# Performance work log

Hardware: AMD Instinct MI355X
Metric: run time of the kernel (lower is better)

## Reference

```python
import jax, jax.numpy as jnp
import numpy as np

N = 12000       # nodes (Hi-C bins, max_num_nodes)
F_IN = 16       # number_genomic_annotations
HID = 4 * F_IN  # conv1 out = 64
NCLUST = 100    # n_clust
E = 384000      # edges (avg degree 32)


def setup_inputs() -> dict:
    key = jax.random.key(0)
    ks = jax.random.split(key, 8)
    x = jax.random.normal(ks[0], (N, F_IN), dtype=jnp.float32)
    edge_index = jax.random.randint(ks[1], (2, E), 0, N)
    edge_attr = jax.random.uniform(ks[2], (E,), dtype=jnp.float32)
    s1 = 1.0 / np.sqrt(F_IN)
    W1_rel = jax.random.uniform(ks[3], (HID, F_IN), minval=-s1, maxval=s1, dtype=jnp.float32)
    W1_root = jax.random.uniform(ks[4], (HID, F_IN), minval=-s1, maxval=s1, dtype=jnp.float32)
    b1 = jnp.zeros((HID,), jnp.float32)
    s2 = 1.0 / np.sqrt(HID)
    W2_rel = jax.random.uniform(ks[5], (NCLUST, HID), minval=-s2, maxval=s2, dtype=jnp.float32)
    W2_root = jax.random.uniform(ks[6], (NCLUST, HID), minval=-s2, maxval=s2, dtype=jnp.float32)
    b2 = jnp.zeros((NCLUST,), jnp.float32)
    return dict(x=x, edge_index=edge_index, edge_attr=edge_attr,
                W1_rel=W1_rel, W1_root=W1_root, b1=b1,
                W2_rel=W2_rel, W2_root=W2_root, b2=b2)


def _graph_conv(x, src, dst, ew, W_rel, W_root, b):
    # PyG GraphConv (aggr='add'): out = lin_rel(sum_j e_ji * x_j) + lin_root(x)
    msg = x[src] * ew[:, None]                       # [E, F]
    aggr = jax.ops.segment_sum(msg, dst, num_segments=N)  # [N, F]
    return aggr @ W_rel.T + b + x @ W_root.T


def reference(x, edge_index, edge_attr, W1_rel, W1_root, b1, W2_rel, W2_root, b2):
    src, dst = edge_index[0], edge_index[1]
    h = _graph_conv(x, src, dst, edge_attr, W1_rel, W1_root, b1)
    h = jax.nn.relu(h)  # dropout is identity in eval mode
    s_out = _graph_conv(h, src, dst, edge_attr, W2_rel, W2_root, b2)  # [N, NCLUST]

    # to_dense_adj (duplicate edges summed)
    adj = jnp.zeros((N, N), x.dtype).at[src, dst].add(edge_attr)  # [N, N]

    # dense_mincut_pool with S = x (as in the original forward), k = F_IN
    s_mc = jax.nn.softmax(x, axis=-1)      # [N, F_IN]
    as_ = adj @ s_mc                        # [N, F_IN]
    out_adj = s_mc.T @ as_                  # [F_IN, F_IN]
    mincut_num = jnp.trace(out_adj)
    d_flat = adj.sum(-1)                    # [N] degree
    mincut_den = jnp.einsum('ik,i,ik->', s_mc, d_flat, s_mc)  # trace(S^T D S)
    mc = -(mincut_num / mincut_den)

    ss = s_mc.T @ s_mc                      # [F_IN, F_IN]
    i_k = jnp.eye(F_IN, dtype=ss.dtype)
    o = jnp.linalg.norm(ss / jnp.linalg.norm(ss) - i_k / jnp.linalg.norm(i_k))

    return jax.nn.softmax(s_out, axis=-1), mc, o
```

## Files before the change

### kernel.cpp

```cpp
#include <hip/hip_runtime.h>
#include <math.h>

#define N_NODES 12000
#define F_INN 16
#define HIDD 64
#define NCLUST 100
#define NEDGE 384000
#define NBLK_N 47
#define CAP 96
#define EPT 4
#define NBLK_E 375
#define NBLK_F1 (N_NODES / 4)
#define NBLK_F2 (N_NODES / 8)

#define OFF_COUNT   0
#define OFF_SCAL    12000
#define ZERO_ELEMS  12002
#define OFF_SSPART  12004
#define OFF_NORM2   24036
#define OFF_W2TREL  36036
#define OFF_W2TROOT 42436
#define OFF_SMC     48836
#define OFF_H       240836
#define OFF_SRCW    1008836

__global__ void zero_kernel(int* __restrict__ ws) {
    int i = blockIdx.x * 256 + threadIdx.x;
    if (i < ZERO_ELEMS) ws[i] = 0;
}

__global__ void phase0_kernel(const float* __restrict__ x, const int* __restrict__ ei,
                              const float* __restrict__ ew, float* __restrict__ smc,
                              float* __restrict__ norm2, int* __restrict__ count,
                              int2* __restrict__ srcw, const float* __restrict__ W2_rel,
                              const float* __restrict__ W2_root, float* __restrict__ w2t_rel,
                              float* __restrict__ w2t_root) {
    __shared__ float fl[6400];
    int t = threadIdx.x;
    int b = blockIdx.x;
    if (b < NBLK_N) {
        int i = b * 256 + t;
        if (i >= N_NODES) return;
        const float4* xr = (const float4*)(x + i * 16);
        float4 r0 = xr[0], r1 = xr[1], r2 = xr[2], r3 = xr[3];
        float v[16] = {r0.x, r0.y, r0.z, r0.w, r1.x, r1.y, r1.z, r1.w,
                       r2.x, r2.y, r2.z, r2.w, r3.x, r3.y, r3.z, r3.w};
        float m = v[0];
#pragma unroll
        for (int k = 1; k < 16; ++k) m = fmaxf(m, v[k]);
        float s = 0.f;
#pragma unroll
        for (int k = 0; k < 16; ++k) { v[k] = __expf(v[k] - m); s += v[k]; }
        float inv = 1.f / s;
        float n2 = 0.f;
#pragma unroll
        for (int k = 0; k < 16; ++k) { v[k] *= inv; n2 += v[k] * v[k]; }
        float4* so = (float4*)(smc + i * 16);
        so[0] = make_float4(v[0], v[1], v[2], v[3]);
        so[1] = make_float4(v[4], v[5], v[6], v[7]);
        so[2] = make_float4(v[8], v[9], v[10], v[11]);
        so[3] = make_float4(v[12], v[13], v[14], v[15]);
        norm2[i] = n2;
    } else if (b < NBLK_N + NBLK_E) {
        int tid = (b - NBLK_N) * 256 + t;
        int e0 = tid * EPT;
        int4 sv = *(const int4*)(ei + e0);
        int4 dv = *(const int4*)(ei + NEDGE + e0);
        float4 wv = *(const float4*)(ew + e0);
        int s[EPT] = {sv.x, sv.y, sv.z, sv.w};
        int d[EPT] = {dv.x, dv.y, dv.z, dv.w};
        float w[EPT] = {wv.x, wv.y, wv.z, wv.w};
        int pos[EPT];
#pragma unroll
        for (int i = 0; i < EPT; ++i) pos[i] = atomicAdd(&count[d[i]], 1);
#pragma unroll
        for (int i = 0; i < EPT; ++i) {
            unsigned long long pv = ((unsigned long long)(unsigned)__float_as_int(w[i]) << 32) |
                                    (unsigned)s[i];
            __builtin_nontemporal_store(pv, (unsigned long long*)&srcw[d[i] * CAP + pos[i]]);
        }
    } else {
        const float* src = (b == NBLK_N + NBLK_E) ? W2_rel : W2_root;
        float* dst = (b == NBLK_N + NBLK_E) ? w2t_rel : w2t_root;
        for (int i = t; i < 6400; i += 256) fl[i] = src[i];
        __syncthreads();
        for (int j = t; j < 6400; j += 256) {
            int kk = j / 100, cl = j - kk * 100;
            dst[j] = fl[cl * 64 + kk];
        }
    }
}

__global__ void fused1_pass2_kernel(const float* __restrict__ x, const int2* __restrict__ srcw,
                                    const int* __restrict__ count, const float* __restrict__ W1_rel,
                                    const float* __restrict__ W1_root, const float* __restrict__ b1,
                                    float* __restrict__ h, const float* __restrict__ smc,
                                    float* __restrict__ sspart, const int* __restrict__ ei,
                                    const float* __restrict__ ew, const float* __restrict__ norm2,
                                    float* __restrict__ scal) {
    __shared__ float shm[4352];
    int t = threadIdx.x;
    int b = blockIdx.x;
    if (b < NBLK_F1) {
        float* wrelT  = shm;
        float* wrootT = shm + 1024;
        float* b1s    = shm + 2048;
        float* aggr   = shm + 2112;
        float* xs     = shm + 2176;
        for (int idx = t; idx < 1024; idx += 256) {
            int f = idx >> 4, k = idx & 15;
            wrelT[(k << 6) + f]  = W1_rel[idx];
            wrootT[(k << 6) + f] = W1_root[idx];
        }
        if (t < 64) b1s[t] = b1[t];
        int w = t >> 6, lane = t & 63;
        int j2 = lane >> 2;
        int q  = lane & 3;
        int n = b * 4 + w;
        int len = count[n];
        const int2* bucket = srcw + n * CAP;
        float4 acc4 = make_float4(0.f, 0.f, 0.f, 0.f);
        int k = 0;
        for (; k + 31 < len; k += 32) {
            int2 pa = bucket[k + j2];
            int2 pb = bucket[k + 16 + j2];
            float4 va = *(const float4*)(x + pa.x * 16 + q * 4);
            float4 vb = *(const float4*)(x + pb.x * 16 + q * 4);
            float wa = __int_as_float(pa.y), wb = __int_as_float(pb.y);
            acc4.x = fmaf(va.x, wa, acc4.x); acc4.y = fmaf(va.y, wa, acc4.y);
            acc4.z = fmaf(va.z, wa, acc4.z); acc4.w = fmaf(va.w, wa, acc4.w);
            acc4.x = fmaf(vb.x, wb, acc4.x); acc4.y = fmaf(vb.y, wb, acc4.y);
            acc4.z = fmaf(vb.z, wb, acc4.z); acc4.w = fmaf(vb.w, wb, acc4.w);
        }
        for (; k < len; k += 16) {
            if (k + j2 < len) {
                int2 p = bucket[k + j2];
                float4 v = *(const float4*)(x + p.x * 16 + q * 4);
                float wt = __int_as_float(p.y);
                acc4.x = fmaf(v.x, wt, acc4.x); acc4.y = fmaf(v.y, wt, acc4.y);
                acc4.z = fmaf(v.z, wt, acc4.z); acc4.w = fmaf(v.w, wt, acc4.w);
            }
        }
        acc4.x += __shfl_xor(acc4.x, 4);  acc4.y += __shfl_xor(acc4.y, 4);
        acc4.z += __shfl_xor(acc4.z, 4);  acc4.w += __shfl_xor(acc4.w, 4);
        acc4.x += __shfl_xor(acc4.x, 8);  acc4.y += __shfl_xor(acc4.y, 8);
        acc4.z += __shfl_xor(acc4.z, 8);  acc4.w += __shfl_xor(acc4.w, 8);
        acc4.x += __shfl_xor(acc4.x, 16); acc4.y += __shfl_xor(acc4.y, 16);
        acc4.z += __shfl_xor(acc4.z, 16); acc4.w += __shfl_xor(acc4.w, 16);
        acc4.x += __shfl_xor(acc4.x, 32); acc4.y += __shfl_xor(acc4.y, 32);
        acc4.z += __shfl_xor(acc4.z, 32); acc4.w += __shfl_xor(acc4.w, 32);
        if (j2 == 0) *(float4*)(aggr + w * 16 + q * 4) = acc4;
        if (lane < 16) xs[w * 16 + lane] = x[n * 16 + lane];
        __syncthreads();
        float o = b1s[lane];
#pragma unroll
        for (int kk = 0; kk < 16; ++kk)
            o = fmaf(aggr[w * 16 + kk], wrelT[(kk << 6) + lane],
                     fmaf(xs[w * 16 + kk], wrootT[(kk << 6) + lane], o));
        __builtin_nontemporal_store(fmaxf(o, 0.f), &h[n * 64 + lane]);
    } else if (b < NBLK_F1 + NBLK_N) {
        int bb = b - NBLK_F1;
        float* rows = shm;
        int n = bb * 256 + t;
        float* rp = rows + t * 17;
        if (n < N_NODES) {
            const float4* sr = (const float4*)(smc + n * 16);
            float4 a0 = sr[0], a1 = sr[1], a2v = sr[2], a3 = sr[3];
            rp[0] = a0.x;  rp[1] = a0.y;  rp[2] = a0.z;  rp[3] = a0.w;
            rp[4] = a1.x;  rp[5] = a1.y;  rp[6] = a1.z;  rp[7] = a1.w;
            rp[8] = a2v.x; rp[9] = a2v.y; rp[10] = a2v.z; rp[11] = a2v.w;
            rp[12] = a3.x; rp[13] = a3.y; rp[14] = a3.z; rp[15] = a3.w;
        } else {
#pragma unroll
            for (int k = 0; k < 16; ++k) rp[k] = 0.f;
        }
        __syncthreads();
        int a = t & 15, bq = t >> 4;
        float accs = 0.f;
#pragma unroll 4
        for (int r = 0; r < 256; ++r)
            accs = fmaf(rows[r * 17 + a], rows[r * 17 + bq], accs);
        sspart[bb * 256 + t] = accs;
    } else {
        int tid = (b - NBLK_F1 - NBLK_N) * 256 + t;
        int e0 = tid * EPT;
        int4 sv = *(const int4*)(ei + e0);
        int4 dv = *(const int4*)(ei + NEDGE + e0);
        float4 wv = *(const float4*)(ew + e0);
        int s[EPT] = {sv.x, sv.y, sv.z, sv.w};
        int d[EPT] = {dv.x, dv.y, dv.z, dv.w};
        float w[EPT] = {wv.x, wv.y, wv.z, wv.w};
        float np = 0.f, dp = 0.f;
#pragma unroll
        for (int i = 0; i < EPT; ++i) {
            const float4* ps = (const float4*)(smc + s[i] * 16);
            const float4* pd = (const float4*)(smc + d[i] * 16);
            float4 s0 = ps[0], s1 = ps[1], s2 = ps[2], s3 = ps[3];
            float4 d0 = pd[0], d1 = pd[1], d2 = pd[2], d3 = pd[3];
            float dot = s0.x * d0.x + s0.y * d0.y + s0.z * d0.z + s0.w * d0.w +
                        s1.x * d1.x + s1.y * d1.y + s1.z * d1.z + s1.w * d1.w +
                        s2.x * d2.x + s2.y * d2.y + s2.z * d2.z + s2.w * d2.w +
                        s3.x * d3.x + s3.y * d3.y + s3.z * d3.z + s3.w * d3.w;
            np = fmaf(w[i], dot, np);
            dp = fmaf(w[i], norm2[s[i]], dp);
        }
        float* redn = shm;
        float* redd = shm + 256;
        redn[t] = np;
        redd[t] = dp;
        __syncthreads();
        for (int s2 = 128; s2 > 0; s2 >>= 1) {
            if (t < s2) { redn[t] += redn[t + s2]; redd[t] += redd[t + s2]; }
            __syncthreads();
        }
        if (t == 0) {
            atomicAdd(&scal[0], redn[0]);
            atomicAdd(&scal[1], redd[0]);
        }
    }
}

__global__ __launch_bounds__(512) void fused2_finalize_kernel(
    const float* __restrict__ h, const int2* __restrict__ srcw, const int* __restrict__ count,
    const float* __restrict__ w2t_rel, const float* __restrict__ w2t_root,
    const float* __restrict__ b2, float* __restrict__ out, const float* __restrict__ sspart,
    const float* __restrict__ scal) {
    __shared__ float wsrel[6400];
    __shared__ float a2[8][64], hrow[8][64];
    __shared__ float logits[8][104];
    __shared__ float b2s[104];
    int t = threadIdx.x;
    int b = blockIdx.x;
    if (b < NBLK_F2) {
        for (int i = t; i < 6400; i += 512) wsrel[i] = w2t_rel[i];
        if (t < NCLUST) b2s[t] = b2[t];
        int nn = t >> 6;
        int c = t & 63;
        int eslot = c >> 4;
        int q = c & 15;
        int n = b * 8 + nn;
        int len = count[n];
        const int2* bucket = srcw + n * CAP;
        float4 acc4 = make_float4(0.f, 0.f, 0.f, 0.f);
        int k = 0;
        for (; k + 31 < len; k += 32) {
            int2 pa = bucket[k + eslot];
            int2 pb = bucket[k + 4 + eslot];
            int2 pc = bucket[k + 8 + eslot];
            int2 pd = bucket[k + 12 + eslot];
            int2 pe = bucket[k + 16 + eslot];
            int2 pf = bucket[k + 20 + eslot];
            int2 pg = bucket[k + 24 + eslot];
            int2 ph = bucket[k + 28 + eslot];
            float4 va = *(const float4*)(h + pa.x * 64 + q * 4);
            float4 vb = *(const float4*)(h + pb.x * 64 + q * 4);
            float4 vc = *(const float4*)(h + pc.x * 64 + q * 4);
            float4 vd = *(const float4*)(h + pd.x * 64 + q * 4);
            float4 ve = *(const float4*)(h + pe.x * 64 + q * 4);
            float4 vf = *(const float4*)(h + pf.x * 64 + q * 4);
            float4 vg = *(const float4*)(h + pg.x * 64 + q * 4);
            float4 vh = *(const float4*)(h + ph.x * 64 + q * 4);
            float wa = __int_as_float(pa.y), wb = __int_as_float(pb.y);
            float wc = __int_as_float(pc.y), wd = __int_as_float(pd.y);
            float we = __int_as_float(pe.y), wf = __int_as_float(pf.y);
            float wg = __int_as_float(pg.y), wh = __int_as_float(ph.y);
            acc4.x = fmaf(va.x, wa, acc4.x); acc4.y = fmaf(va.y, wa, acc4.y);
            acc4.z = fmaf(va.z, wa, acc4.z); acc4.w = fmaf(va.w, wa, acc4.w);
            acc4.x = fmaf(vb.x, wb, acc4.x); acc4.y = fmaf(vb.y, wb, acc4.y);
            acc4.z = fmaf(vb.z, wb, acc4.z); acc4.w = fmaf(vb.w, wb, acc4.w);
            acc4.x = fmaf(vc.x, wc, acc4.x); acc4.y = fmaf(vc.y, wc, acc4.y);
            acc4.z = fmaf(vc.z, wc, acc4.z); acc4.w = fmaf(vc.w, wc, acc4.w);
            acc4.x = fmaf(vd.x, wd, acc4.x); acc4.y = fmaf(vd.y, wd, acc4.y);
            acc4.z = fmaf(vd.z, wd, acc4.z); acc4.w = fmaf(vd.w, wd, acc4.w);
            acc4.x = fmaf(ve.x, we, acc4.x); acc4.y = fmaf(ve.y, we, acc4.y);
            acc4.z = fmaf(ve.z, we, acc4.z); acc4.w = fmaf(ve.w, we, acc4.w);
            acc4.x = fmaf(vf.x, wf, acc4.x); acc4.y = fmaf(vf.y, wf, acc4.y);
            acc4.z = fmaf(vf.z, wf, acc4.z); acc4.w = fmaf(vf.w, wf, acc4.w);
            acc4.x = fmaf(vg.x, wg, acc4.x); acc4.y = fmaf(vg.y, wg, acc4.y);
            acc4.z = fmaf(vg.z, wg, acc4.z); acc4.w = fmaf(vg.w, wg, acc4.w);
            acc4.x = fmaf(vh.x, wh, acc4.x); acc4.y = fmaf(vh.y, wh, acc4.y);
            acc4.z = fmaf(vh.z, wh, acc4.z); acc4.w = fmaf(vh.w, wh, acc4.w);
        }
        for (; k < len; k += 4) {
            if (k + eslot < len) {
                int2 p = bucket[k + eslot];
                float4 v = *(const float4*)(h + p.x * 64 + q * 4);
                float wt = __int_as_float(p.y);
                acc4.x = fmaf(v.x, wt, acc4.x); acc4.y = fmaf(v.y, wt, acc4.y);
                acc4.z = fmaf(v.z, wt, acc4.z); acc4.w = fmaf(v.w, wt, acc4.w);
            }
        }
        acc4.x += __shfl_xor(acc4.x, 16); acc4.y += __shfl_xor(acc4.y, 16);
        acc4.z += __shfl_xor(acc4.z, 16); acc4.w += __shfl_xor(acc4.w, 16);
        acc4.x += __shfl_xor(acc4.x, 32); acc4.y += __shfl_xor(acc4.y, 32);
        acc4.z += __shfl_xor(acc4.z, 32); acc4.w += __shfl_xor(acc4.w, 32);
        if (eslot == 0) *(float4*)(&a2[nn][q * 4]) = acc4;
        hrow[nn][c] = h[n * 64 + c];
        __syncthreads();
        int g = t >> 7, c2 = t & 127;
        if (c2 < NCLUST) {
            int na = 2 * g, nb2 = 2 * g + 1;
            float s0 = b2s[c2], s1 = s0;
#pragma unroll 8
            for (int kk = 0; kk < 64; ++kk) {
                float wr = wsrel[kk * 100 + c2];
                float wo = w2t_root[kk * 100 + c2];
                s0 = fmaf(a2[na][kk], wr, fmaf(hrow[na][kk], wo, s0));
                s1 = fmaf(a2[nb2][kk], wr, fmaf(hrow[nb2][kk], wo, s1));
            }
            logits[na][c2] = s0;
            logits[nb2][c2] = s1;
        }
        __syncthreads();
        float v0 = logits[nn][c];
        float v1 = (c < NCLUST - 64) ? logits[nn][64 + c] : -INFINITY;
        float m = fmaxf(v0, v1);
#pragma unroll
        for (int off = 32; off > 0; off >>= 1) m = fmaxf(m, __shfl_xor(m, off));
        float e0 = __expf(v0 - m);
        float e1 = (c < NCLUST - 64) ? __expf(v1 - m) : 0.f;
        float s = e0 + e1;
#pragma unroll
        for (int off = 32; off > 0; off >>= 1) s += __shfl_xor(s, off);
        float inv = 1.f / s;
        out[n * NCLUST + c] = e0 * inv;
        if (c < NCLUST - 64) out[n * NCLUST + 64 + c] = e1 * inv;
    } else {
        float* red = wsrel;
        float sv = 0.f;
        if (t < 256)
            for (int bb = 0; bb < NBLK_N; ++bb) sv += sspart[bb * 256 + t];
        red[t] = sv * sv;
        __syncthreads();
        for (int s = 256; s > 0; s >>= 1) {
            if (t < s) red[t] += red[t + s];
            __syncthreads();
        }
        float ssnorm = sqrtf(red[0]);
        __syncthreads();
        float diff = (t < 256) ? (sv / ssnorm - ((t % 17 == 0) ? 0.25f : 0.f)) : 0.f;
        red[t] = diff * diff;
        __syncthreads();
        for (int s = 256; s > 0; s >>= 1) {
            if (t < s) red[t] += red[t + s];
            __syncthreads();
        }
        if (t == 0) {
            out[N_NODES * NCLUST + 0] = -(scal[0] / scal[1]);
            out[N_NODES * NCLUST + 1] = sqrtf(red[0]);
        }
    }
}

extern "C" void kernel_launch(void* const* d_in, const int* in_sizes, int n_in,
                              void* d_out, int out_size, void* d_ws, size_t ws_size,
                              hipStream_t stream) {
    const float* x       = (const float*)d_in[0];
    const int*   ei      = (const int*)d_in[1];
    const float* ew      = (const float*)d_in[2];
    const float* W1_rel  = (const float*)d_in[3];
    const float* W1_root = (const float*)d_in[4];
    const float* b1      = (const float*)d_in[5];
    const float* W2_rel  = (const float*)d_in[6];
    const float* W2_root = (const float*)d_in[7];
    const float* b2      = (const float*)d_in[8];
    float* out = (float*)d_out;
    int*   wsi = (int*)d_ws;

    int*   count   = wsi + OFF_COUNT;
    float* scal    = (float*)(wsi + OFF_SCAL);
    float* sspart  = (float*)(wsi + OFF_SSPART);
    float* norm2   = (float*)(wsi + OFF_NORM2);
    float* w2trel  = (float*)(wsi + OFF_W2TREL);
    float* w2troot = (float*)(wsi + OFF_W2TROOT);
    float* smc     = (float*)(wsi + OFF_SMC);
    float* h       = (float*)(wsi + OFF_H);
    int2*  srcw    = (int2*)(wsi + OFF_SRCW);

    zero_kernel<<<(ZERO_ELEMS + 255) / 256, 256, 0, stream>>>(wsi);
    phase0_kernel<<<NBLK_N + NBLK_E + 2, 256, 0, stream>>>(x, ei, ew, smc, norm2, count, srcw,
                                                           W2_rel, W2_root, w2trel, w2troot);
    fused1_pass2_kernel<<<NBLK_F1 + NBLK_N + NBLK_E, 256, 0, stream>>>(
        x, srcw, count, W1_rel, W1_root, b1, h, smc, sspart, ei, ew, norm2, scal);
    fused2_finalize_kernel<<<NBLK_F2 + 1, 512, 0, stream>>>(h, srcw, count, w2trel, w2troot,
                                                            b2, out, sspart, scal);
}
```

Measured before the change: 102.9 us.

## Drop W2 transpose staging and double block size of fused pass kernel

Removes the W2 transpose blocks from phase0. The second-layer matvec now reads W2_rel/W2_root row-major through float4 global loads instead of copying a 25KB transposed weight tile into LDS in every block, which cuts shared-memory staging and the LDS footprint per block. The fused layer-1/mincut kernel moves to 512-thread blocks: 8 nodes per block, a larger reduction and a bounds check for the edge-reduction blocks. The trade is more L1/L2 traffic for the weights and idle half-blocks in the sspart section.

```diff
diff --git a/kernel.cpp b/kernel.cpp
--- a/kernel.cpp
+++ b/kernel.cpp
@@ -10,7 +10,8 @@
 #define CAP 96
 #define EPT 4
 #define NBLK_E 375
-#define NBLK_F1 (N_NODES / 4)
+#define NBLK_F1 (N_NODES / 8)
+#define NBLK_ME 188
 #define NBLK_F2 (N_NODES / 8)
 
 #define OFF_COUNT   0
@@ -18,8 +19,6 @@
 #define ZERO_ELEMS  12002
 #define OFF_SSPART  12004
 #define OFF_NORM2   24036
-#define OFF_W2TREL  36036
-#define OFF_W2TROOT 42436
 #define OFF_SMC     48836
 #define OFF_H       240836
 #define OFF_SRCW    1008836
@@ -32,10 +31,7 @@
 __global__ void phase0_kernel(const float* __restrict__ x, const int* __restrict__ ei,
                               const float* __restrict__ ew, float* __restrict__ smc,
                               float* __restrict__ norm2, int* __restrict__ count,
-                              int2* __restrict__ srcw, const float* __restrict__ W2_rel,
-                              const float* __restrict__ W2_root, float* __restrict__ w2t_rel,
-                              float* __restrict__ w2t_root) {
-    __shared__ float fl[6400];
+                              int2* __restrict__ srcw) {
     int t = threadIdx.x;
     int b = blockIdx.x;
     if (b < NBLK_N) {
@@ -61,7 +57,7 @@
         so[2] = make_float4(v[8], v[9], v[10], v[11]);
         so[3] = make_float4(v[12], v[13], v[14], v[15]);
         norm2[i] = n2;
-    } else if (b < NBLK_N + NBLK_E) {
+    } else {
         int tid = (b - NBLK_N) * 256 + t;
         int e0 = tid * EPT;
         int4 sv = *(const int4*)(ei + e0);
@@ -79,25 +75,15 @@
                                     (unsigned)s[i];
             __builtin_nontemporal_store(pv, (unsigned long long*)&srcw[d[i] * CAP + pos[i]]);
         }
-    } else {
-        const float* src = (b == NBLK_N + NBLK_E) ? W2_rel : W2_root;
-        float* dst = (b == NBLK_N + NBLK_E) ? w2t_rel : w2t_root;
-        for (int i = t; i < 6400; i += 256) fl[i] = src[i];
-        __syncthreads();
-        for (int j = t; j < 6400; j += 256) {
-            int kk = j / 100, cl = j - kk * 100;
-            dst[j] = fl[cl * 64 + kk];
-        }
     }
 }
 
-__global__ void fused1_pass2_kernel(const float* __restrict__ x, const int2* __restrict__ srcw,
-                                    const int* __restrict__ count, const float* __restrict__ W1_rel,
-                                    const float* __restrict__ W1_root, const float* __restrict__ b1,
-                                    float* __restrict__ h, const float* __restrict__ smc,
-                                    float* __restrict__ sspart, const int* __restrict__ ei,
-                                    const float* __restrict__ ew, const float* __restrict__ norm2,
-                                    float* __restrict__ scal) {
+__global__ __launch_bounds__(512) void fused1_pass2_kernel(
+    const float* __restrict__ x, const int2* __restrict__ srcw, const int* __restrict__ count,
+    const float* __restrict__ W1_rel, const float* __restrict__ W1_root,
+    const float* __restrict__ b1, float* __restrict__ h, const float* __restrict__ smc,
+    float* __restrict__ sspart, const int* __restrict__ ei, const float* __restrict__ ew,
+    const float* __restrict__ norm2, float* __restrict__ scal) {
     __shared__ float shm[4352];
     int t = threadIdx.x;
     int b = blockIdx.x;
@@ -106,8 +92,8 @@
         float* wrootT = shm + 1024;
         float* b1s    = shm + 2048;
         float* aggr   = shm + 2112;
-        float* xs     = shm + 2176;
-        for (int idx = t; idx < 1024; idx += 256) {
+        float* xs     = shm + 2240;
+        for (int idx = t; idx < 1024; idx += 512) {
             int f = idx >> 4, k = idx & 15;
             wrelT[(k << 6) + f]  = W1_rel[idx];
             wrootT[(k << 6) + f] = W1_root[idx];
@@ -116,7 +102,7 @@
         int w = t >> 6, lane = t & 63;
         int j2 = lane >> 2;
         int q  = lane & 3;
-        int n = b * 4 + w;
+        int n = b * 8 + w;
         int len = count[n];
         const int2* bucket = srcw + n * CAP;
         float4 acc4 = make_float4(0.f, 0.f, 0.f, 0.f);
@@ -162,54 +148,60 @@
         int bb = b - NBLK_F1;
         float* rows = shm;
         int n = bb * 256 + t;
-        float* rp = rows + t * 17;
-        if (n < N_NODES) {
-            const float4* sr = (const float4*)(smc + n * 16);
-            float4 a0 = sr[0], a1 = sr[1], a2v = sr[2], a3 = sr[3];
-            rp[0] = a0.x;  rp[1] = a0.y;  rp[2] = a0.z;  rp[3] = a0.w;
-            rp[4] = a1.x;  rp[5] = a1.y;  rp[6] = a1.z;  rp[7] = a1.w;
-            rp[8] = a2v.x; rp[9] = a2v.y; rp[10] = a2v.z; rp[11] = a2v.w;
-            rp[12] = a3.x; rp[13] = a3.y; rp[14] = a3.z; rp[15] = a3.w;
-        } else {
-#pragma unroll
-            for (int k = 0; k < 16; ++k) rp[k] = 0.f;
-        }
-        __syncthreads();
-        int a = t & 15, bq = t >> 4;
-        float accs = 0.f;
+        if (t < 256) {
+            float* rp = rows + t * 17;
+            if (n < N_NODES) {
+                const float4* sr = (const float4*)(smc + n * 16);
+                float4 a0 = sr[0], a1 = sr[1], a2v = sr[2], a3 = sr[3];
+                rp[0] = a0.x;  rp[1] = a0.y;  rp[2] = a0.z;  rp[3] = a0.w;
+                rp[4] = a1.x;  rp[5] = a1.y;  rp[6] = a1.z;  rp[7] = a1.w;
+                rp[8] = a2v.x; rp[9] = a2v.y; rp[10] = a2v.z; rp[11] = a2v.w;
+                rp[12] = a3.x; rp[13] = a3.y; rp[14] = a3.z; rp[15] = a3.w;
+            } else {
+#pragma unroll
+                for (int k = 0; k < 16; ++k) rp[k] = 0.f;
+            }
+        }
+        __syncthreads();
+        if (t < 256) {
+            int a = t & 15, bq = t >> 4;
+            float accs = 0.f;
 #pragma unroll 4
-        for (int r = 0; r < 256; ++r)
-            accs = fmaf(rows[r * 17 + a], rows[r * 17 + bq], accs);
-        sspart[bb * 256 + t] = accs;
+            for (int r = 0; r < 256; ++r)
+                accs = fmaf(rows[r * 17 + a], rows[r * 17 + bq], accs);
+            sspart[bb * 256 + t] = accs;
+        }
     } else {
-        int tid = (b - NBLK_F1 - NBLK_N) * 256 + t;
+        int tid = (b - NBLK_F1 - NBLK_N) * 512 + t;
         int e0 = tid * EPT;
-        int4 sv = *(const int4*)(ei + e0);
-        int4 dv = *(const int4*)(ei + NEDGE + e0);
-        float4 wv = *(const float4*)(ew + e0);
-        int s[EPT] = {sv.x, sv.y, sv.z, sv.w};
-        int d[EPT] = {dv.x, dv.y, dv.z, dv.w};
-        float w[EPT] = {wv.x, wv.y, wv.z, wv.w};
         float np = 0.f, dp = 0.f;
-#pragma unroll
-        for (int i = 0; i < EPT; ++i) {
-            const float4* ps = (const float4*)(smc + s[i] * 16);
-            const float4* pd = (const float4*)(smc + d[i] * 16);
-            float4 s0 = ps[0], s1 = ps[1], s2 = ps[2], s3 = ps[3];
-            float4 d0 = pd[0], d1 = pd[1], d2 = pd[2], d3 = pd[3];
-            float dot = s0.x * d0.x + s0.y * d0.y + s0.z * d0.z + s0.w * d0.w +
-                        s1.x * d1.x + s1.y * d1.y + s1.z * d1.z + s1.w * d1.w +
-                        s2.x * d2.x + s2.y * d2.y + s2.z * d2.z + s2.w * d2.w +
-                        s3.x * d3.x + s3.y * d3.y + s3.z * d3.z + s3.w * d3.w;
-            np = fmaf(w[i], dot, np);
-            dp = fmaf(w[i], norm2[s[i]], dp);
+        if (e0 < NEDGE) {
+            int4 sv = *(const int4*)(ei + e0);
+            int4 dv = *(const int4*)(ei + NEDGE + e0);
+            float4 wv = *(const float4*)(ew + e0);
+            int s[EPT] = {sv.x, sv.y, sv.z, sv.w};
+            int d[EPT] = {dv.x, dv.y, dv.z, dv.w};
+            float w[EPT] = {wv.x, wv.y, wv.z, wv.w};
+#pragma unroll
+            for (int i = 0; i < EPT; ++i) {
+                const float4* ps = (const float4*)(smc + s[i] * 16);
+                const float4* pd = (const float4*)(smc + d[i] * 16);
+                float4 s0 = ps[0], s1 = ps[1], s2 = ps[2], s3 = ps[3];
+                float4 d0 = pd[0], d1 = pd[1], d2 = pd[2], d3 = pd[3];
+                float dot = s0.x * d0.x + s0.y * d0.y + s0.z * d0.z + s0.w * d0.w +
+                            s1.x * d1.x + s1.y * d1.y + s1.z * d1.z + s1.w * d1.w +
+                            s2.x * d2.x + s2.y * d2.y + s2.z * d2.z + s2.w * d2.w +
+                            s3.x * d3.x + s3.y * d3.y + s3.z * d3.z + s3.w * d3.w;
+                np = fmaf(w[i], dot, np);
+                dp = fmaf(w[i], norm2[s[i]], dp);
+            }
         }
         float* redn = shm;
-        float* redd = shm + 256;
+        float* redd = shm + 512;
         redn[t] = np;
         redd[t] = dp;
         __syncthreads();
-        for (int s2 = 128; s2 > 0; s2 >>= 1) {
+        for (int s2 = 256; s2 > 0; s2 >>= 1) {
             if (t < s2) { redn[t] += redn[t + s2]; redd[t] += redd[t + s2]; }
             __syncthreads();
         }
@@ -222,17 +214,18 @@
 
 __global__ __launch_bounds__(512) void fused2_finalize_kernel(
     const float* __restrict__ h, const int2* __restrict__ srcw, const int* __restrict__ count,
-    const float* __restrict__ w2t_rel, const float* __restrict__ w2t_root,
+    const float* __restrict__ W2_rel, const float* __restrict__ W2_root,
     const float* __restrict__ b2, float* __restrict__ out, const float* __restrict__ sspart,
     const float* __restrict__ scal) {
-    __shared__ float wsrel[6400];
-    __shared__ float a2[8][64], hrow[8][64];
+    __shared__ float4 a2v[8][16];
+    __shared__ float4 hrowv[8][16];
     __shared__ float logits[8][104];
     __shared__ float b2s[104];
+    float* a2 = (float*)a2v;
+    float* hrow = (float*)hrowv;
     int t = threadIdx.x;
     int b = blockIdx.x;
     if (b < NBLK_F2) {
-        for (int i = t; i < 6400; i += 512) wsrel[i] = w2t_rel[i];
         if (t < NCLUST) b2s[t] = b2[t];
         int nn = t >> 6;
         int c = t & 63;
@@ -294,19 +287,29 @@
         acc4.z += __shfl_xor(acc4.z, 16); acc4.w += __shfl_xor(acc4.w, 16);
         acc4.x += __shfl_xor(acc4.x, 32); acc4.y += __shfl_xor(acc4.y, 32);
         acc4.z += __shfl_xor(acc4.z, 32); acc4.w += __shfl_xor(acc4.w, 32);
-        if (eslot == 0) *(float4*)(&a2[nn][q * 4]) = acc4;
-        hrow[nn][c] = h[n * 64 + c];
+        if (eslot == 0) a2v[nn][q] = acc4;
+        hrow[nn * 64 + c] = h[n * 64 + c];
         __syncthreads();
         int g = t >> 7, c2 = t & 127;
         if (c2 < NCLUST) {
             int na = 2 * g, nb2 = 2 * g + 1;
+            const float4* wr4 = (const float4*)(W2_rel + c2 * 64);
+            const float4* wo4 = (const float4*)(W2_root + c2 * 64);
             float s0 = b2s[c2], s1 = s0;
-#pragma unroll 8
-            for (int kk = 0; kk < 64; ++kk) {
-                float wr = wsrel[kk * 100 + c2];
-                float wo = w2t_root[kk * 100 + c2];
-                s0 = fmaf(a2[na][kk], wr, fmaf(hrow[na][kk], wo, s0));
-                s1 = fmaf(a2[nb2][kk], wr, fmaf(hrow[nb2][kk], wo, s1));
+#pragma unroll 4
+            for (int q4 = 0; q4 < 16; ++q4) {
+                float4 wr = wr4[q4];
+                float4 wo = wo4[q4];
+                float4 aa = a2v[na][q4],  ha = hrowv[na][q4];
+                float4 ab = a2v[nb2][q4], hb = hrowv[nb2][q4];
+                s0 = fmaf(aa.x, wr.x, fmaf(ha.x, wo.x, s0));
+                s1 = fmaf(ab.x, wr.x, fmaf(hb.x, wo.x, s1));
+                s0 = fmaf(aa.y, wr.y, fmaf(ha.y, wo.y, s0));
+                s1 = fmaf(ab.y, wr.y, fmaf(hb.y, wo.y, s1));
+                s0 = fmaf(aa.z, wr.z, fmaf(ha.z, wo.z, s0));
+                s1 = fmaf(ab.z, wr.z, fmaf(hb.z, wo.z, s1));
+                s0 = fmaf(aa.w, wr.w, fmaf(ha.w, wo.w, s0));
+                s1 = fmaf(ab.w, wr.w, fmaf(hb.w, wo.w, s1));
             }
             logits[na][c2] = s0;
             logits[nb2][c2] = s1;
@@ -326,7 +329,7 @@
         out[n * NCLUST + c] = e0 * inv;
         if (c < NCLUST - 64) out[n * NCLUST + 64 + c] = e1 * inv;
     } else {
-        float* red = wsrel;
+        float* red = a2;
         float sv = 0.f;
         if (t < 256)
             for (int bb = 0; bb < NBLK_N; ++bb) sv += sspart[bb * 256 + t];
@@ -371,17 +374,14 @@
     float* scal    = (float*)(wsi + OFF_SCAL);
     float* sspart  = (float*)(wsi + OFF_SSPART);
     float* norm2   = (float*)(wsi + OFF_NORM2);
-    float* w2trel  = (float*)(wsi + OFF_W2TREL);
-    float* w2troot = (float*)(wsi + OFF_W2TROOT);
     float* smc     = (float*)(wsi + OFF_SMC);
     float* h       = (float*)(wsi + OFF_H);
     int2*  srcw    = (int2*)(wsi + OFF_SRCW);
 
     zero_kernel<<<(ZERO_ELEMS + 255) / 256, 256, 0, stream>>>(wsi);
-    phase0_kernel<<<NBLK_N + NBLK_E + 2, 256, 0, stream>>>(x, ei, ew, smc, norm2, count, srcw,
-                                                           W2_rel, W2_root, w2trel, w2troot);
-    fused1_pass2_kernel<<<NBLK_F1 + NBLK_N + NBLK_E, 256, 0, stream>>>(
+    phase0_kernel<<<NBLK_N + NBLK_E, 256, 0, stream>>>(x, ei, ew, smc, norm2, count, srcw);
+    fused1_pass2_kernel<<<NBLK_F1 + NBLK_N + NBLK_ME, 512, 0, stream>>>(
         x, srcw, count, W1_rel, W1_root, b1, h, smc, sspart, ei, ew, norm2, scal);
-    fused2_finalize_kernel<<<NBLK_F2 + 1, 512, 0, stream>>>(h, srcw, count, w2trel, w2troot,
+    fused2_finalize_kernel<<<NBLK_F2 + 1, 512, 0, stream>>>(h, srcw, count, W2_rel, W2_root,
                                                             b2, out, sspart, scal);
 }
```

Result: slower. 126.0 us (+22.5%).
